# Kernel tuning notes

Measured on AMD Instinct MI355X. Metric: run time of the kernel, lower is better.

The kernel has to match this reference:

```python
import jax, jax.numpy as jnp
import numpy as np

CODEBOOK_SIZE = 1024
EMBED_DIM = 256
X_SHAPE = (8, 4, 32, 32, EMBED_DIM)  # [B, T, H, W, C] video latents


def setup_inputs() -> dict:
    key = jax.random.key(0)
    kx, kc = jax.random.split(key)
    x = jax.random.normal(kx, X_SHAPE, dtype=jnp.float32)
    # variance_scaling(scale=1.0, mode='fan_in', distribution='uniform') over (codebook_size, d):
    # fan_in = d, limit = sqrt(3 / fan_in)
    limit = float(np.sqrt(3.0 / EMBED_DIM))
    codebook = jax.random.uniform(kc, (CODEBOOK_SIZE, EMBED_DIM), dtype=jnp.float32,
                                  minval=-limit, maxval=limit)
    return {"x": x, "codebook": codebook}


def reference(x, codebook):
    d = x.shape[-1]
    k = codebook.shape[0]
    flat = x.reshape(-1, d)  # [N, d]
    distances = (jnp.sum(flat * flat, axis=-1, keepdims=True)
                 - 2.0 * jnp.dot(flat, codebook.T)
                 + jnp.sum(codebook * codebook, axis=-1))
    distances = distances.reshape(x.shape[:-1] + (k,))
    encoding_indices = jnp.argmin(distances, axis=-1)  # [...]
    encodings = jax.nn.one_hot(encoding_indices, k, dtype=x.dtype)  # [..., K]
    # quantize: one-hot @ codebook (== gather of codebook rows)
    quantized = jnp.dot(encodings, codebook)  # [..., d]
    return quantized
```

## Files before the change

kernel.cpp:

```cpp
#include <hip/hip_runtime.h>


#define D         256
#define K_TOTAL   1024
#define N_ROWS    32768
#define TM        64
#define TN        64
#define NCHUNK    (K_TOTAL / TN)
#define CS_STRIDE 260

__global__ void norms_kernel(const float* __restrict__ x, const float* __restrict__ cb,
                             float* __restrict__ xnorm, float* __restrict__ cnorm) {
    const int wave = threadIdx.x >> 6;
    const int lane = threadIdx.x & 63;
    const int row  = blockIdx.x * 4 + wave;

    const float* src;
    float* dst;
    int idx;
    if (row < N_ROWS) { src = x  + (size_t)row * D;             dst = xnorm; idx = row; }
    else              { src = cb + (size_t)(row - N_ROWS) * D;  dst = cnorm; idx = row - N_ROWS; }

    float4 v = *(const float4*)(src + lane * 4);
    float sx = v.x * v.x;
    float sy = v.y * v.y;
    float sz = v.z * v.z;
    float sw = v.w * v.w;
    double s = (double)sx + (double)sy + (double)sz + (double)sw;
    #pragma unroll
    for (int off = 32; off > 0; off >>= 1)
        s += __shfl_down(s, off, 64);
    if (lane == 0) dst[idx] = (float)s;
}

__global__ __launch_bounds__(256, 2)
void vq_kernel(const float* __restrict__ x, const float* __restrict__ cb,
               const float* __restrict__ xnorm, const float* __restrict__ cnorm,
               float* __restrict__ out) {
    __shared__ float cs[TN * CS_STRIDE];
    __shared__ float red_val[TM * 16];
    __shared__ int   red_idx[TM * 16];
    __shared__ int   best_idx[TM];

    const int tid = threadIdx.x;
    const int tx  = tid & 15;
    const int ty  = tid >> 4;
    const int n0  = blockIdx.x * TM;

    float runmin[4];
    int   runidx[4];
    float S[4];
    const float* xrow[4];
    #pragma unroll
    for (int i = 0; i < 4; ++i) {
        runmin[i] = 1e30f; runidx[i] = 0;
        const int n = n0 + ty + 16 * i;
        S[i]    = xnorm[n];
        xrow[i] = x + (size_t)n * D;
    }

    for (int kc = 0; kc < NCHUNK; ++kc) {
        const int k0 = kc * TN;

        __syncthreads();
        {
            const int col4 = tid & 63;
            const int row  = tid >> 6;
            #pragma unroll
            for (int r = 0; r < 16; ++r) {
                const int rr = row + 4 * r;
                float4 v = *(const float4*)(cb + (size_t)(k0 + rr) * D + col4 * 4);
                *(float4*)(cs + rr * CS_STRIDE + col4 * 4) = v;
            }
        }
        __syncthreads();

        float acc[4][4];
        #pragma unroll
        for (int i = 0; i < 4; ++i)
            #pragma unroll
            for (int j = 0; j < 4; ++j) acc[i][j] = 0.f;

        #pragma unroll 2
        for (int dd = 0; dd < D; dd += 4) {
            float4 a[4], b[4];
            #pragma unroll
            for (int i = 0; i < 4; ++i) a[i] = *(const float4*)(xrow[i] + dd);
            #pragma unroll
            for (int j = 0; j < 4; ++j) b[j] = *(const float4*)(cs + (tx + 16 * j) * CS_STRIDE + dd);
            #pragma unroll
            for (int i = 0; i < 4; ++i)
                #pragma unroll
                for (int j = 0; j < 4; ++j) {
                    acc[i][j] += a[i].x * b[j].x;
                    acc[i][j] += a[i].y * b[j].y;
                    acc[i][j] += a[i].z * b[j].z;
                    acc[i][j] += a[i].w * b[j].w;
                }
        }

        #pragma unroll
        for (int j = 0; j < 4; ++j) {
            const int k = k0 + tx + 16 * j;
            const float cn = cnorm[k];
            #pragma unroll
            for (int i = 0; i < 4; ++i) {
                const float t = S[i] - 2.0f * acc[i][j];
                const float q = t + cn;
                if (q < runmin[i]) { runmin[i] = q; runidx[i] = k; }
            }
        }
    }

    __syncthreads();
    #pragma unroll
    for (int i = 0; i < 4; ++i) {
        const int row = ty + 16 * i;
        red_val[row * 16 + tx] = runmin[i];
        red_idx[row * 16 + tx] = runidx[i];
    }
    __syncthreads();
    if (tid < TM) {
        const int row = tid;
        float bv = red_val[row * 16];
        int   bi = red_idx[row * 16];
        #pragma unroll
        for (int t = 1; t < 16; ++t) {
            const float v = red_val[row * 16 + t];
            const int  ix = red_idx[row * 16 + t];
            if (v < bv || (v == bv && ix < bi)) { bv = v; bi = ix; }
        }
        best_idx[row] = bi;
    }
    __syncthreads();

    {
        const int col4 = tid & 63;
        const int row  = tid >> 6;
        #pragma unroll
        for (int r = 0; r < 16; ++r) {
            const int rr = row + 4 * r;
            const int k  = best_idx[rr];
            float4 v = *(const float4*)(cb + (size_t)k * D + col4 * 4);
            *(float4*)(out + (size_t)(n0 + rr) * D + col4 * 4) = v;
        }
    }
}

extern "C" void kernel_launch(void* const* d_in, const int* in_sizes, int n_in,
                              void* d_out, int out_size, void* d_ws, size_t ws_size,
                              hipStream_t stream) {
    const float* x  = (const float*)d_in[0];
    const float* cb = (const float*)d_in[1];
    float* out = (float*)d_out;

    float* xnorm = (float*)d_ws;
    float* cnorm = xnorm + N_ROWS;

    norms_kernel<<<(N_ROWS + K_TOTAL) / 4, 256, 0, stream>>>(x, cb, xnorm, cnorm);
    vq_kernel<<<N_ROWS / TM, 256, 0, stream>>>(x, cb, xnorm, cnorm, out);
}
```

Measured before the change: 372.3 us.

## Stage x tile in LDS, stream codebook from global, fuse x-norm into VQ kernel

The roles of the operands are swapped. The 64-row x tile is now loaded once into shared memory, and codebook rows are read straight from global memory (L2-resident) in groups of 8 per thread. This removes the per-chunk shared-memory staging and the two block-wide barriers for each of the 16 codebook chunks. The x row norms are now computed inside the VQ kernel from the staged tile, so the separate norm pass over x is dropped. The register tile grows from 4x4 to 4x8 accumulators, which may raise register pressure, and codebook reads now depend on global/L2 bandwidth instead of LDS.

```diff
diff --git a/kernel.cpp b/kernel.cpp
--- a/kernel.cpp
+++ b/kernel.cpp
@@ -5,93 +5,99 @@
 #define K_TOTAL   1024
 #define N_ROWS    32768
 #define TM        64
-#define TN        64
-#define NCHUNK    (K_TOTAL / TN)
-#define CS_STRIDE 260
+#define XS_STRIDE 260
 
-__global__ void norms_kernel(const float* __restrict__ x, const float* __restrict__ cb,
-                             float* __restrict__ xnorm, float* __restrict__ cnorm) {
+__global__ void cnorm_kernel(const float* __restrict__ cb, float* __restrict__ cnorm) {
     const int wave = threadIdx.x >> 6;
     const int lane = threadIdx.x & 63;
-    const int row  = blockIdx.x * 4 + wave;
-
-    const float* src;
-    float* dst;
-    int idx;
-    if (row < N_ROWS) { src = x  + (size_t)row * D;             dst = xnorm; idx = row; }
-    else              { src = cb + (size_t)(row - N_ROWS) * D;  dst = cnorm; idx = row - N_ROWS; }
-
-    float4 v = *(const float4*)(src + lane * 4);
-    float sx = v.x * v.x;
-    float sy = v.y * v.y;
-    float sz = v.z * v.z;
-    float sw = v.w * v.w;
+    const int k    = blockIdx.x * 4 + wave;
+    float4 v = *(const float4*)(cb + (size_t)k * D + lane * 4);
+    float sx = v.x * v.x, sy = v.y * v.y, sz = v.z * v.z, sw = v.w * v.w;
     double s = (double)sx + (double)sy + (double)sz + (double)sw;
     #pragma unroll
     for (int off = 32; off > 0; off >>= 1)
         s += __shfl_down(s, off, 64);
-    if (lane == 0) dst[idx] = (float)s;
+    if (lane == 0) cnorm[k] = (float)s;
 }
 
 __global__ __launch_bounds__(256, 2)
 void vq_kernel(const float* __restrict__ x, const float* __restrict__ cb,
-               const float* __restrict__ xnorm, const float* __restrict__ cnorm,
-               float* __restrict__ out) {
-    __shared__ float cs[TN * CS_STRIDE];
-    __shared__ float red_val[TM * 16];
-    __shared__ int   red_idx[TM * 16];
-    __shared__ int   best_idx[TM];
+               const float* __restrict__ cnorm, float* __restrict__ out) {
+    __shared__ float  xs[TM * XS_STRIDE];
+    __shared__ double sred[TM][4];
+    __shared__ float  red_val[TM * 16];
+    __shared__ int    red_idx[TM * 16];
+    __shared__ int    best_idx[TM];
 
     const int tid = threadIdx.x;
     const int tx  = tid & 15;
     const int ty  = tid >> 4;
     const int n0  = blockIdx.x * TM;
 
+    #pragma unroll
+    for (int r = 0; r < 16; ++r) {
+        const int idx  = tid + 256 * r;
+        const int row  = idx >> 6;
+        const int col4 = idx & 63;
+        float4 v = *(const float4*)(x + (size_t)(n0 + row) * D + col4 * 4);
+        *(float4*)(xs + row * XS_STRIDE + col4 * 4) = v;
+    }
+    __syncthreads();
+
+    {
+        const int r = tid >> 2, seg = tid & 3;
+        const float* p = xs + r * XS_STRIDE + seg * 64;
+        double s = 0.0;
+        #pragma unroll
+        for (int d = 0; d < 64; d += 4) {
+            float4 v = *(const float4*)(p + d);
+            float a0 = v.x * v.x, a1 = v.y * v.y, a2 = v.z * v.z, a3 = v.w * v.w;
+            s += (double)a0 + (double)a1 + (double)a2 + (double)a3;
+        }
+        sred[r][seg] = s;
+    }
+    __syncthreads();
+
+    float S[4];
+    const float* arow[4];
+    #pragma unroll
+    for (int i = 0; i < 4; ++i) {
+        const int rr = ty + 16 * i;
+        S[i]    = (float)(sred[rr][0] + sred[rr][1] + sred[rr][2] + sred[rr][3]);
+        arow[i] = xs + rr * XS_STRIDE;
+    }
+
     float runmin[4];
     int   runidx[4];
-    float S[4];
-    const float* xrow[4];
     #pragma unroll
-    for (int i = 0; i < 4; ++i) {
-        runmin[i] = 1e30f; runidx[i] = 0;
-        const int n = n0 + ty + 16 * i;
-        S[i]    = xnorm[n];
-        xrow[i] = x + (size_t)n * D;
-    }
+    for (int i = 0; i < 4; ++i) { runmin[i] = 1e30f; runidx[i] = 0; }
 
-    for (int kc = 0; kc < NCHUNK; ++kc) {
-        const int k0 = kc * TN;
+    for (int jg = 0; jg < 8; ++jg) {
+        int kk[8];
+        const float* brow[8];
+        #pragma unroll
+        for (int j = 0; j < 8; ++j) {
+            kk[j]   = tx + 16 * (8 * jg + j);
+            brow[j] = cb + (size_t)kk[j] * D;
+        }
 
-        __syncthreads();
-        {
-            const int col4 = tid & 63;
-            const int row  = tid >> 6;
-            #pragma unroll
-            for (int r = 0; r < 16; ++r) {
-                const int rr = row + 4 * r;
-                float4 v = *(const float4*)(cb + (size_t)(k0 + rr) * D + col4 * 4);
-                *(float4*)(cs + rr * CS_STRIDE + col4 * 4) = v;
-            }
-        }
-        __syncthreads();
-
-        float acc[4][4];
+        float acc[4][8];
         #pragma unroll
         for (int i = 0; i < 4; ++i)
             #pragma unroll
-            for (int j = 0; j < 4; ++j) acc[i][j] = 0.f;
+            for (int j = 0; j < 8; ++j) acc[i][j] = 0.f;
 
         #pragma unroll 2
         for (int dd = 0; dd < D; dd += 4) {
-            float4 a[4], b[4];
+            float4 b[8], a[4];
             #pragma unroll
-            for (int i = 0; i < 4; ++i) a[i] = *(const float4*)(xrow[i] + dd);
+            for (int j = 0; j < 8; ++j) b[j] = *(const float4*)(brow[j] + dd);
             #pragma unroll
-            for (int j = 0; j < 4; ++j) b[j] = *(const float4*)(cs + (tx + 16 * j) * CS_STRIDE + dd);
+            for (int i = 0; i < 4; ++i) a[i] = *(const float4*)(arow[i] + dd);
             #pragma unroll
             for (int i = 0; i < 4; ++i)
                 #pragma unroll
-                for (int j = 0; j < 4; ++j) {
+                for (int j = 0; j < 8; ++j) {
                     acc[i][j] += a[i].x * b[j].x;
                     acc[i][j] += a[i].y * b[j].y;
                     acc[i][j] += a[i].z * b[j].z;
@@ -100,14 +106,13 @@
         }
 
         #pragma unroll
-        for (int j = 0; j < 4; ++j) {
-            const int k = k0 + tx + 16 * j;
-            const float cn = cnorm[k];
+        for (int j = 0; j < 8; ++j) {
+            const float cn = cnorm[kk[j]];
             #pragma unroll
             for (int i = 0; i < 4; ++i) {
                 const float t = S[i] - 2.0f * acc[i][j];
                 const float q = t + cn;
-                if (q < runmin[i]) { runmin[i] = q; runidx[i] = k; }
+                if (q < runmin[i]) { runmin[i] = q; runidx[i] = kk[j]; }
             }
         }
     }
@@ -152,11 +157,10 @@
                               hipStream_t stream) {
     const float* x  = (const float*)d_in[0];
     const float* cb = (const float*)d_in[1];
-    float* out = (float*)d_out;
+    float* out   = (float*)d_out;
+    float* cnorm = (float*)d_ws;
 
-    float* xnorm = (float*)d_ws;
-    float* cnorm = xnorm + N_ROWS;
-
-    norms_kernel<<<(N_ROWS + K_TOTAL) / 4, 256, 0, stream>>>(x, cb, xnorm, cnorm);
-    vq_kernel<<<N_ROWS / TM, 256, 0, stream>>>(x, cb, xnorm, cnorm, out);
+    const int N = in_sizes[0] / D;
+    cnorm_kernel<<<K_TOTAL / 4, 256, 0, stream>>>(cb, cnorm);
+    vq_kernel<<<N / TM, 256, 0, stream>>>(x, cb, cnorm, out);
 }
```

After: 977.4 us. +162.5%, slower.
